# Kernel optimization log

Hardware: AMD Instinct MI355X
Metric: run time of the kernel (lower is better)

Reference implementation:

```python
import math
import jax, jax.numpy as jnp
import numpy as np

CELL = 16
BLOCK = 2
NBINS = 9


def setup_inputs() -> dict:
    key = jax.random.key(0)
    im = jax.random.normal(key, (16, 3, 512, 512), dtype=jnp.float32)
    return {"im": im}


def _l2hys(x):
    # L2 normalize over (bh, bw, bins), clamp at 0.2, renormalize (L2-Hys)
    n1 = jnp.sqrt(jnp.sum(x * x, axis=(-1, -2, -3), keepdims=True))
    t = jnp.minimum(x / (n1 + 1e-10), 0.2)
    n2 = jnp.sqrt(jnp.sum(t * t, axis=(-1, -2, -3), keepdims=True))
    return t / (n2 + 1e-10)


def _hog_forward(im):
    B, C, H, W = im.shape
    cs, nb, bs = CELL, NBINS, BLOCK
    gain = nb / math.pi
    # complex Sobel kernel: real part = x-gradient, imag part = y-gradient
    kx = jnp.array([[-1., 0., 1.], [-2., 0., 2.], [-1., 0., 1.]], jnp.float32)
    ky = jnp.array([[-1., -2., -1.], [0., 0., 0.], [1., 2., 1.]], jnp.float32)
    imp = jnp.pad(im, ((0, 0), (0, 0), (1, 1), (1, 1)), mode="reflect")
    x = imp.reshape(B * C, 1, H + 2, W + 2)
    k = jnp.stack([kx, ky])[:, None]  # (2,1,3,3)
    g = jax.lax.conv_general_dilated(x, k, (1, 1), "VALID")  # (B*C,2,H,W) cross-correlation, matches F.conv2d
    gx = g[:, 0].reshape(B, C, H, W)
    gy = g[:, 1].reshape(B, C, H, W)
    Hc, Wc = H // cs, W // cs
    P = cs * cs

    def unfold_cells(a):  # (B,C,H,W) -> (B,C,Hc,Wc,cs*cs)
        return a.reshape(B, C, Hc, cs, Wc, cs).transpose(0, 1, 2, 4, 3, 5).reshape(B, C, Hc, Wc, P)

    gx = unfold_cells(gx)
    gy = unfold_cells(gy)
    norm = jnp.sqrt(gx * gx + gy * gy)  # complex magnitude
    # channelWise=False: pick the channel with max magnitude per pixel
    idx = jnp.argmax(norm, axis=1, keepdims=True)
    norm = jnp.take_along_axis(norm, idx, axis=1)
    gx = jnp.take_along_axis(gx, idx, axis=1)
    gy = jnp.take_along_axis(gy, idx, axis=1)
    phase = jnp.mod(jnp.arctan2(gy, gx), math.pi)  # complex angle mod pi

    # bilinear soft binning via scatter_add
    edges = jnp.linspace(0.0, math.pi, nb + 1)
    left = jnp.floor(gain * phase).astype(jnp.int32)
    prct = gain * (phase - edges[left])
    li = left % nb
    ri = (left + 1) % nb
    N = B * 1 * Hc * Wc
    rows = jnp.broadcast_to(jnp.arange(N)[:, None], (N, P))
    hist = jnp.zeros((N, nb), norm.dtype)
    hist = hist.at[rows, li.reshape(N, P)].add(((1.0 - prct) * norm).reshape(N, P))
    hist = hist.at[rows, ri.reshape(N, P)].add((prct * norm).reshape(N, P))
    hist = hist.reshape(B, 1, Hc, Wc, nb) / float(P)

    # block normalize: unfold cells into overlapping blocks (stride = blockSize//2)
    step = bs // 2
    Hb = (Hc - bs) // step + 1
    Wb = (Wc - bs) // step + 1
    blocks = jnp.stack(
        [
            jnp.stack(
                [hist[:, :, i:i + step * (Hb - 1) + 1:step, j:j + step * (Wb - 1) + 1:step, :] for j in range(bs)],
                axis=-2,
            )
            for i in range(bs)
        ],
        axis=-3,
    )  # (B,1,Hb,Wb,bs,bs,nb)
    return _l2hys(blocks)


def reference(im):
    return _hog_forward(im)
```

## Files before the change

### kernel.cpp

```cpp
#include <hip/hip_runtime.h>
#include <hip/hip_bf16.h>
#include <math.h>


#define IMG_H 512
#define IMG_W 512
#define NCH 3
#define NB_ 16
#define HC 32
#define WC 32
#define HB 31
#define WB 31
#define NBINS 9

__device__ __forceinline__ int refl(int i, int n) {
    if (i < 0) i = -i;
    else if (i >= n) i = 2 * n - 2 - i;
    return i;
}

__global__ __launch_bounds__(256) void hog_hist_kernel(const float* __restrict__ im,
                                                       float* __restrict__ hist) {
    const int bid = blockIdx.x;
    const int b  = bid >> 7;
    const int tr = (bid >> 4) & 7;
    const int tc = bid & 15;

    const int t  = threadIdx.x;
    const int cg = t & 7;
    const int rg = t >> 3;

    const int y0 = tr * 64 + rg * 2;
    const int x0 = tc * 32 + cg * 4;

    const float* imb = im + (size_t)b * NCH * IMG_H * IMG_W;

    int yoff[4];
#pragma unroll
    for (int j = 0; j < 4; ++j) yoff[j] = refl(y0 - 1 + j, IMG_H) * IMG_W;
    const int xl = (x0 == 0) ? 1 : x0 - 1;
    const int xr = (x0 + 4 >= IMG_W) ? IMG_W - 2 : x0 + 4;

    float be[8], bgx[8], bgy[8];

#pragma unroll
    for (int c = 0; c < NCH; ++c) {
        const float* chp = imb + (size_t)c * (IMG_H * IMG_W);
        float w[4][6];
#pragma unroll
        for (int j = 0; j < 4; ++j) {
            const float* rp = chp + yoff[j];
            const float4 v = *(const float4*)(rp + x0);
            w[j][0] = rp[xl];
            w[j][1] = v.x; w[j][2] = v.y; w[j][3] = v.z; w[j][4] = v.w;
            w[j][5] = rp[xr];
        }
#pragma unroll
        for (int p = 0; p < 2; ++p) {
#pragma unroll
            for (int q = 0; q < 4; ++q) {
                const int ix = p * 4 + q;
                float gx = ((w[p][q + 2] - w[p][q]) + 2.0f * (w[p + 1][q + 2] - w[p + 1][q]))
                         + (w[p + 2][q + 2] - w[p + 2][q]);
                float gy = ((w[p + 2][q] - w[p][q]) + 2.0f * (w[p + 2][q + 1] - w[p][q + 1]))
                         + (w[p + 2][q + 2] - w[p][q + 2]);
                float e = gx * gx + gy * gy;
                if (c == 0) {
                    be[ix] = e; bgx[ix] = gx; bgy[ix] = gy;
                } else {
                    bool gt = e > be[ix];
                    be[ix]  = gt ? e  : be[ix];
                    bgx[ix] = gt ? gx : bgx[ix];
                    bgy[ix] = gt ? gy : bgy[ix];
                }
            }
        }
    }

    const float PI_F  = (float)M_PI;
    const float HPI_F = (float)(M_PI / 2.0);
    const float GAIN  = (float)(9.0 / M_PI);
    const float C1  = 0.99997726f, C3 = -0.33262347f, C5 = 0.19354346f;
    const float C7  = -0.11643287f, C9 = 0.05265332f, C11 = -0.01172120f;

    float acc[NBINS];
#pragma unroll
    for (int k = 0; k < NBINS; ++k) acc[k] = 0.0f;

#pragma unroll
    for (int p = 0; p < 8; ++p) {
        float gx = bgx[p], gy = bgy[p];
        float n = __builtin_amdgcn_sqrtf(be[p]);
        float ax = fabsf(gx), ay = fabsf(gy);
        float mn = fminf(ax, ay), mx = fmaxf(ax, ay);
        float r  = mn * __builtin_amdgcn_rcpf(mx + 1e-37f);
        float r2 = r * r;
        float at = r * (C1 + r2 * (C3 + r2 * (C5 + r2 * (C7 + r2 * (C9 + r2 * C11)))));
        if (ay > ax) at = HPI_F - at;
        if ((__float_as_uint(gx) ^ __float_as_uint(gy)) & 0x80000000u) at = PI_F - at;
        float fp = GAIN * at;

        float w0 = fmaxf(1.0f - fabsf(fp), 0.0f) + fmaxf(1.0f - fabsf(fp - 9.0f), 0.0f);
        acc[0] = fmaf(w0, n, acc[0]);
#pragma unroll
        for (int k = 1; k < NBINS; ++k) {
            float wk = fmaxf(1.0f - fabsf(fp - (float)k), 0.0f);
            acc[k] = fmaf(wk, n, acc[k]);
        }
    }

#pragma unroll
    for (int k = 0; k < NBINS; ++k) acc[k] += __shfl_xor(acc[k], 1, 64);
#pragma unroll
    for (int k = 0; k < NBINS; ++k) acc[k] += __shfl_xor(acc[k], 2, 64);
#pragma unroll
    for (int k = 0; k < NBINS; ++k) acc[k] += __shfl_xor(acc[k], 8, 64);
#pragma unroll
    for (int k = 0; k < NBINS; ++k) acc[k] += __shfl_xor(acc[k], 16, 64);
#pragma unroll
    for (int k = 0; k < NBINS; ++k) acc[k] += __shfl_xor(acc[k], 32, 64);

    const int lane = t & 63;
    if ((lane & 0x3B) == 0) {
        const int cellX = tc * 2 + (lane >> 2);
        const int cellY = tr * 4 + (t >> 6);
        float* hp = hist + (((size_t)b * HC + cellY) * WC + cellX) * NBINS;
#pragma unroll
        for (int k = 0; k < NBINS; ++k) hp[k] = acc[k] * (1.0f / 256.0f);
    }
}

__global__ __launch_bounds__(256) void hog_norm_kernel(const float* __restrict__ hist,
                                                       float* __restrict__ out) {
    int idx = blockIdx.x * 256 + threadIdx.x;
    if (idx >= NB_ * HB * WB) return;
    int b = idx / (HB * WB);
    int r = idx - b * (HB * WB);
    int i = r / WB;
    int j = r - i * WB;

    float v[36];
    float ss = 0.0f;
#pragma unroll
    for (int bi = 0; bi < 2; ++bi) {
#pragma unroll
        for (int bj = 0; bj < 2; ++bj) {
            const float* hp = hist + (size_t)(((b * HC) + (i + bi)) * WC + (j + bj)) * NBINS;
#pragma unroll
            for (int k = 0; k < NBINS; ++k) {
                float x = hp[k];
                v[(bi * 2 + bj) * NBINS + k] = x;
                ss += x * x;
            }
        }
    }
    float inv1 = 1.0f / (sqrtf(ss) + 1e-10f);
    float ss2 = 0.0f;
#pragma unroll
    for (int k = 0; k < 36; ++k) {
        float tt = fminf(v[k] * inv1, 0.2f);
        v[k] = tt;
        ss2 += tt * tt;
    }
    float inv2 = 1.0f / (sqrtf(ss2) + 1e-10f);
    float* op = out + (size_t)idx * 36;
#pragma unroll
    for (int k = 0; k < 36; ++k) op[k] = v[k] * inv2;
}

extern "C" void kernel_launch(void* const* d_in, const int* in_sizes, int n_in,
                              void* d_out, int out_size, void* d_ws, size_t ws_size,
                              hipStream_t stream) {
    const float* im = (const float*)d_in[0];
    float* out = (float*)d_out;
    float* hist = (float*)d_ws;

    hog_hist_kernel<<<NB_ * 8 * 16, 256, 0, stream>>>(im, hist);

    int nout_blocks = NB_ * HB * WB;
    hog_norm_kernel<<<(nout_blocks + 255) / 256, 256, 0, stream>>>(hist, out);
}
```

Measured before the change: 33.77 us.

## Map one wavefront per block in norm kernel, swizzle hist block order

```diff
diff --git a/kernel.cpp b/kernel.cpp
--- a/kernel.cpp
+++ b/kernel.cpp
@@ -21,7 +21,7 @@
 
 __global__ __launch_bounds__(256) void hog_hist_kernel(const float* __restrict__ im,
                                                        float* __restrict__ hist) {
-    const int bid = blockIdx.x;
+    const int bid = (int)(((blockIdx.x & 7) << 8) | (blockIdx.x >> 3));
     const int b  = bid >> 7;
     const int tr = (bid >> 4) & 7;
     const int tc = bid & 15;
@@ -100,11 +100,11 @@
         if ((__float_as_uint(gx) ^ __float_as_uint(gy)) & 0x80000000u) at = PI_F - at;
         float fp = GAIN * at;
 
-        float w0 = fmaxf(1.0f - fabsf(fp), 0.0f) + fmaxf(1.0f - fabsf(fp - 9.0f), 0.0f);
+        float w0 = __saturatef(1.0f - fp) + __saturatef(fp - 8.0f);
         acc[0] = fmaf(w0, n, acc[0]);
 #pragma unroll
         for (int k = 1; k < NBINS; ++k) {
-            float wk = fmaxf(1.0f - fabsf(fp - (float)k), 0.0f);
+            float wk = __saturatef(1.0f - fabsf(fp - (float)k));
             acc[k] = fmaf(wk, n, acc[k]);
         }
     }
@@ -132,40 +132,37 @@
 
 __global__ __launch_bounds__(256) void hog_norm_kernel(const float* __restrict__ hist,
                                                        float* __restrict__ out) {
-    int idx = blockIdx.x * 256 + threadIdx.x;
-    if (idx >= NB_ * HB * WB) return;
-    int b = idx / (HB * WB);
-    int r = idx - b * (HB * WB);
-    int i = r / WB;
-    int j = r - i * WB;
+    const int t    = threadIdx.x;
+    const int wv   = t >> 6;
+    const int lane = t & 63;
+    const int idx  = blockIdx.x * 4 + wv;
 
-    float v[36];
-    float ss = 0.0f;
+    const int b = idx / (HB * WB);
+    const int r = idx - b * (HB * WB);
+    const int i = r / WB;
+    const int j = r - i * WB;
+
+    float x = 0.0f;
+    if (lane < 36) {
+        const int cellIdx = lane / NBINS;
+        const int bin     = lane - cellIdx * NBINS;
+        const int bi = cellIdx >> 1;
+        const int bj = cellIdx & 1;
+        x = hist[(size_t)(((b * HC) + (i + bi)) * WC + (j + bj)) * NBINS + bin];
+    }
+
+    float ss = x * x;
 #pragma unroll
-    for (int bi = 0; bi < 2; ++bi) {
+    for (int m = 1; m <= 32; m <<= 1) ss += __shfl_xor(ss, m, 64);
+    const float inv1 = 1.0f / (sqrtf(ss) + 1e-10f);
+
+    const float tt = fminf(x * inv1, 0.2f);
+    float ss2 = tt * tt;
 #pragma unroll
-        for (int bj = 0; bj < 2; ++bj) {
-            const float* hp = hist + (size_t)(((b * HC) + (i + bi)) * WC + (j + bj)) * NBINS;
-#pragma unroll
-            for (int k = 0; k < NBINS; ++k) {
-                float x = hp[k];
-                v[(bi * 2 + bj) * NBINS + k] = x;
-                ss += x * x;
-            }
-        }
-    }
-    float inv1 = 1.0f / (sqrtf(ss) + 1e-10f);
-    float ss2 = 0.0f;
-#pragma unroll
-    for (int k = 0; k < 36; ++k) {
-        float tt = fminf(v[k] * inv1, 0.2f);
-        v[k] = tt;
-        ss2 += tt * tt;
-    }
-    float inv2 = 1.0f / (sqrtf(ss2) + 1e-10f);
-    float* op = out + (size_t)idx * 36;
-#pragma unroll
-    for (int k = 0; k < 36; ++k) op[k] = v[k] * inv2;
+    for (int m = 1; m <= 32; m <<= 1) ss2 += __shfl_xor(ss2, m, 64);
+    const float inv2 = 1.0f / (sqrtf(ss2) + 1e-10f);
+
+    if (lane < 36) out[(size_t)idx * 36 + lane] = tt * inv2;
 }
 
 extern "C" void kernel_launch(void* const* d_in, const int* in_sizes, int n_in,
@@ -178,5 +175,5 @@
     hog_hist_kernel<<<NB_ * 8 * 16, 256, 0, stream>>>(im, hist);
 
     int nout_blocks = NB_ * HB * WB;
-    hog_norm_kernel<<<(nout_blocks + 255) / 256, 256, 0, stream>>>(hist, out);
+    hog_norm_kernel<<<nout_blocks / 4, 256, 0, stream>>>(hist, out);
 }
```

Result: faster. 29.96 us (-11.3%).
